# Kernel optimization log

Measured on AMD Instinct MI355X. Metric: run time of the kernel, lower is better.

Reference implementation:

```python
import jax, jax.numpy as jnp
import numpy as np


def _box_iou(a, b):
    # a: [K,4], b: [K,4] in ltrb; returns [K,K] pairwise IoU (torchvision box_iou math)
    area_a = jnp.clip(a[:, 2] - a[:, 0], 0) * jnp.clip(a[:, 3] - a[:, 1], 0)
    area_b = jnp.clip(b[:, 2] - b[:, 0], 0) * jnp.clip(b[:, 3] - b[:, 1], 0)
    lt = jnp.maximum(a[:, None, :2], b[None, :, :2])
    rb = jnp.minimum(a[:, None, 2:], b[None, :, 2:])
    wh = jnp.clip(rb - lt, 0)
    inter = wh[..., 0] * wh[..., 1]
    return inter / (area_a[:, None] + area_b[None, :] - inter + 1e-9)


def _nms_class(score, boxes, th_c, nms_th, K):
    # score: [N], boxes: [N,4]. Keep boxes with score > th_c, take top-K by score,
    # then greedy NMS suppressing lower-scored boxes with IoU >= nms_th (original keeps iou < nms_th).
    masked = jnp.where(score > th_c, score, -jnp.inf)
    top_s, idx = jax.lax.top_k(masked, K)          # descending score order
    valid = top_s > -jnp.inf
    bk = boxes[idx]                                 # [K,4]
    iou = _box_iou(bk, bk)                          # [K,K]
    order = jnp.arange(K)

    def body(alive, i):
        keep_i = alive[i]
        suppress = keep_i & (iou[i] >= nms_th) & (order > i)
        return alive & ~suppress, keep_i

    _, keep = jax.lax.scan(body, valid, order)
    return jnp.where(keep[:, None], bk, 0.0), jnp.where(keep, top_s, 0.0), keep


def decode(bboxes_in, scores_in, dboxes_xywh, conf_th, nms_th, max_num, scale_xy, scale_wh):
    B, C = bboxes_in.shape[0], scores_in.shape[1]
    K = int(max_num)
    # scale_back_batch: xywh offsets -> ltrb absolute boxes, softmax over classes
    b = jnp.transpose(bboxes_in, (0, 2, 1))                         # [B,N,4]
    xy = scale_xy * b[..., :2] * dboxes_xywh[..., 2:] + dboxes_xywh[..., :2]
    wh = jnp.exp(scale_wh * b[..., 2:]) * dboxes_xywh[..., 2:]
    ltrb = jnp.concatenate([xy - 0.5 * wh, xy + 0.5 * wh], axis=-1)  # [B,N,4]
    probs = jax.nn.softmax(jnp.transpose(scores_in, (0, 2, 1)), axis=-1)  # [B,N,C]
    cls_scores = jnp.transpose(probs[..., 1:], (0, 2, 1))            # [B,C-1,N] (skip background cls 0)

    def per_image(scores_cn, boxes_n4):
        f = jax.vmap(lambda s, t: _nms_class(s, boxes_n4, t, nms_th, K))
        return f(scores_cn, conf_th)

    bk, sk, keep = jax.vmap(per_image)(cls_scores, ltrb)  # [B,C-1,K,4], [B,C-1,K], [B,C-1,K]
    M = (C - 1) * K
    labels = jnp.arange(1, C, dtype=jnp.float32)[None, :, None] * keep.astype(jnp.float32)
    return (bk.reshape(B, M, 4), labels.reshape(B, M), sk.reshape(B, M), keep.reshape(B, M))


def setup_inputs() -> dict:
    key = jax.random.key(0)
    k0, k1, k2, k3, k4 = jax.random.split(key, 5)
    B, N, C = 32, 24564, 21
    bboxes_in = 0.5 * jax.random.normal(k0, (B, 4, N), jnp.float32)
    scores_in = jax.random.normal(k1, (B, C, N), jnp.float32)
    cxy = jax.random.uniform(k2, (1, N, 2), jnp.float32)
    dwh = jax.random.uniform(k3, (1, N, 2), jnp.float32, 0.05, 0.5)
    dboxes_xywh = jnp.concatenate([cxy, dwh], axis=-1)
    conf_th = jax.random.uniform(k4, (C - 1,), jnp.float32, 0.01, 0.05)
    return {
        'bboxes_in': bboxes_in,
        'scores_in': scores_in,
        'dboxes_xywh': dboxes_xywh,
        'conf_th': conf_th,
        'nms_th': jnp.float32(0.5),
        'max_num': 200,
        'scale_xy': 0.1,
        'scale_wh': 0.2,
    }


def reference(bboxes_in, scores_in, dboxes_xywh, conf_th, nms_th, max_num, scale_xy, scale_wh):
    # Padded, jit-compatible equivalent of the torch Decoder: per image we return
    # [(C-1)*K] slots of (boxes, labels, scores) with a boolean keep-mask; the torch
    # version returns only the kept (variable-length) entries, in the same order.
    return decode(bboxes_in, scores_in, dboxes_xywh, conf_th, nms_th, max_num, scale_xy, scale_wh)
```

## Files before the change

### kernel.cpp

```cpp
#include <hip/hip_runtime.h>
#include <math.h>

typedef unsigned int uint;
typedef unsigned short u16;
typedef unsigned long long u64;

#define NT 256
#define KTOP 200
#define CAP 256
#define CAPC 3072
#define SEGS 4
#define SEGCAP 512
#define NCLS 21
#define C1 20
#define MROWS 208
#define NSPLIT 48

__device__ __forceinline__ u64 flip64(double d) {
  u64 u = (u64)__double_as_longlong(d);
  return (u & 0x8000000000000000ULL) ? ~u : (u | 0x8000000000000000ULL);
}

__device__ __forceinline__ double unflip64(u64 k) {
  u64 u = (k & 0x8000000000000000ULL) ? (k ^ 0x8000000000000000ULL) : ~k;
  return __longlong_as_double((long long)u);
}

__device__ __forceinline__ uint q_key16(float sf) {
  float qf = (sf + 16.0f) * 4096.0f;
  qf = fmaxf(fminf(qf, 65535.0f), 1.0f);
  return (uint)qf;
}

__device__ __forceinline__ void par_walk(const uint* hist, uint* scan, u64* wm,
                                         uint* res, uint rank, int tid) {
  scan[tid] = hist[tid];
  __syncthreads();
#pragma unroll
  for (int off = 1; off < 256; off <<= 1) {
    uint v = scan[tid];
    uint a = (tid + off < 256) ? scan[tid + off] : 0u;
    __syncthreads();
    scan[tid] = v + a;
    __syncthreads();
  }
  u64 m = __ballot(scan[tid] >= rank);
  if ((tid & 63) == 0) wm[tid >> 6] = m;
  __syncthreads();
  if (tid == 0) {
    int bin = 0;
    for (int w = 3; w >= 0; --w) {
      if (wm[w]) { bin = w * 64 + (63 - __clzll(wm[w])); break; }
    }
    res[0] = (uint)bin;
    res[1] = scan[bin];
    res[2] = hist[bin];
  }
  __syncthreads();
}

__global__ __launch_bounds__(NT) void zero_ghist(uint* __restrict__ g) {
  g[(size_t)blockIdx.x * NT + threadIdx.x] = 0;
}

__global__ __launch_bounds__(NT) void prep_kernel(
    const float* __restrict__ scores, const float* __restrict__ conf_th,
    double* __restrict__ lse_out, u16* __restrict__ keys_out,
    uint* __restrict__ ghist,
    int B, int N, int npad, int perblk)
{
  __shared__ double s_logth[C1];
  __shared__ uint lhist[C1 * 256];
  int tid = threadIdx.x;
  if (tid < C1) s_logth[tid] = log((double)conf_th[tid]);
  for (int i = tid; i < C1 * 256; i += NT) lhist[i] = 0;
  __syncthreads();

  int b = blockIdx.x / NSPLIT, j = blockIdx.x - b * NSPLIT;
  int s0 = j * perblk, e0 = min(N, s0 + perblk);
  int half = (e0 - s0) >> 1;

  for (int p = tid; p < half; p += NT) {
    int n = s0 + 2 * p;
    const float* sc = scores + (size_t)b * NCLS * N + n;
    float2 v[NCLS];
    float mx0 = -INFINITY, mx1 = -INFINITY;
#pragma unroll
    for (int c = 0; c < NCLS; ++c) {
      float2 t = *reinterpret_cast<const float2*>(sc + (size_t)c * N);
      v[c] = t;
      mx0 = fmaxf(mx0, t.x);
      mx1 = fmaxf(mx1, t.y);
    }
    double a0 = 0.0, a1 = 0.0, a2 = 0.0;
    double b0 = 0.0, b1 = 0.0, b2 = 0.0;
#pragma unroll
    for (int c = 0; c < NCLS; ++c) {
      float e0f = __expf(v[c].x - mx0);
      float e1f = __expf(v[c].y - mx1);
      if ((c % 3) == 0)      { a0 += (double)e0f; b0 += (double)e1f; }
      else if ((c % 3) == 1) { a1 += (double)e0f; b1 += (double)e1f; }
      else                   { a2 += (double)e0f; b2 += (double)e1f; }
    }
    double lse0 = (double)mx0 + log(a0 + a1 + a2);
    double lse1 = (double)mx1 + log(b0 + b1 + b2);
    double2 lw; lw.x = lse0; lw.y = lse1;
    reinterpret_cast<double2*>(lse_out + (size_t)b * N + n)[0] = lw;

#pragma unroll
    for (int c = 0; c < C1; ++c) {
      double s0d = (double)v[c + 1].x - lse0;
      double s1d = (double)v[c + 1].y - lse1;
      uint k0 = 0, k1 = 0;
      if (s0d > s_logth[c]) k0 = q_key16((float)s0d);
      if (s1d > s_logth[c]) k1 = q_key16((float)s1d);
      *reinterpret_cast<uint*>(keys_out + ((size_t)b * C1 + c) * npad + n)
          = k0 | (k1 << 16);
      if (k0) atomicAdd(&lhist[c * 256 + (k0 >> 8)], 1u);
      if (k1) atomicAdd(&lhist[c * 256 + (k1 >> 8)], 1u);
    }
  }
  if (j == NSPLIT - 1 && npad > N) {
    int pad = npad - N;
    for (int t = tid; t < pad * C1; t += NT) {
      int c = t / pad, n = N + (t - c * pad);
      keys_out[((size_t)b * C1 + c) * npad + n] = 0;
    }
  }
  __syncthreads();
  for (int i = tid; i < C1 * 256; i += NT) {
    uint v2 = lhist[i];
    if (v2) atomicAdd(&ghist[((size_t)b * C1 + (i >> 8)) * 256 + (i & 255)], v2);
  }
}

__global__ __launch_bounds__(NT) void collect_kernel(
    const u16* __restrict__ keys, const uint* __restrict__ ghist,
    uint4* __restrict__ L0cnt, uint* __restrict__ cand, uint* __restrict__ cnts,
    int npad)
{
  int blk = blockIdx.x;
  int task = blk >> 2, seg = blk & (SEGS - 1);
  int tid = threadIdx.x, lane = tid & 63;
  __shared__ uint sL, sCnt0, sCnt;

  if (tid < 64) {
    uint4 h = reinterpret_cast<const uint4*>(ghist + (size_t)task * 256)[tid];
    uint s = h.x + h.y + h.z + h.w;
    uint suf = s;
#pragma unroll
    for (int off = 1; off < 64; off <<= 1) {
      uint o = (uint)__shfl_down((int)suf, off);
      if (lane + off < 64) suf += o;
    }
    uint total = (uint)__shfl((int)suf, 0);
    uint sn = (uint)__shfl_down((int)suf, 1);
    if (lane == 63) sn = 0;
    uint c3 = h.w + sn, c2 = c3 + h.z, c1 = c2 + h.y, c0 = c1 + h.x;
    uint binoff, cnt, abv;
    if (c3 >= KTOP)      { binoff = 3; cnt = c3; abv = c3 - h.w; }
    else if (c2 >= KTOP) { binoff = 2; cnt = c2; abv = c2 - h.z; }
    else if (c1 >= KTOP) { binoff = 1; cnt = c1; abv = c1 - h.y; }
    else                 { binoff = 0; cnt = c0; abv = c0 - h.x; }
    uint L0v, cnt0v, abovev;
    if (total < KTOP) {
      L0v = 1u; cnt0v = total; abovev = 0u;
    } else {
      u64 m = __ballot(suf >= KTOP);
      int l = 63 - __clzll(m);
      uint bo = (uint)__shfl((int)binoff, l);
      cnt0v = (uint)__shfl((int)cnt, l);
      abovev = (uint)__shfl((int)abv, l);
      L0v = ((uint)(4 * l) + bo) << 8;
    }
    if (lane == 0) {
      sL = L0v; sCnt0 = cnt0v;
      if (seg == 0) L0cnt[task] = make_uint4(L0v, cnt0v, abovev, total);
    }
  }
  if (tid == NT - 1) sCnt = 0;
  __syncthreads();

  uint L = sL, cnt0 = sCnt0;
  if (cnt0 > CAPC) { if (tid == 0) cnts[blk] = 0; return; }

  const u16* krow = keys + (size_t)task * npad;
  const uint4* krow8 = reinterpret_cast<const uint4*>(krow);
  int nv8 = npad >> 3;
  int per8 = (nv8 + SEGS - 1) >> 2;
  int s8 = seg * per8, e8 = min(nv8, s8 + per8);
  uint* myc = cand + ((size_t)task * SEGS + seg) * SEGCAP;

  for (int i = s8 + tid; i < e8; i += NT) {
    uint4 kv = krow8[i];
    uint base = (uint)(i << 3);
    uint ks[8] = { kv.x & 0xFFFFu, kv.x >> 16, kv.y & 0xFFFFu, kv.y >> 16,
                   kv.z & 0xFFFFu, kv.z >> 16, kv.w & 0xFFFFu, kv.w >> 16 };
#pragma unroll
    for (int comp = 0; comp < 8; ++comp) {
      uint k = ks[comp];
      bool f = (k >= L);
      u64 m = __ballot(f);
      if (m) {
        uint nb = (uint)__popcll(m);
        uint wb = 0;
        if (lane == 0) wb = atomicAdd(&sCnt, nb);
        wb = (uint)__shfl((int)wb, 0);
        if (f) {
          uint pos = wb + (uint)__popcll(m & ((1ULL << lane) - 1ULL));
          if (pos < SEGCAP) myc[pos] = (k << 15) | (base + comp);
        }
      }
    }
  }
  __syncthreads();
  if (tid == 0) cnts[blk] = sCnt;
}

__global__ __launch_bounds__(NT) void final_kernel(
    const u16* __restrict__ keys, const uint4* __restrict__ L0cnt,
    const uint* __restrict__ candg, const uint* __restrict__ cnts,
    const float* __restrict__ scores, const double* __restrict__ lse,
    const float* __restrict__ bboxes, const float* __restrict__ dboxes,
    const float* __restrict__ scale_xy_p, const float* __restrict__ scale_wh_p,
    const float* __restrict__ nms_th_p,
    float* __restrict__ out, int B, int N, int npad)
{
  int task = blockIdx.x;
  int b = task / C1, c = task - b * C1;
  int tid = threadIdx.x, lane = tid & 63, wav = tid >> 6;
  const u16* krow = keys + (size_t)task * npad;
  int nv8 = npad >> 3;

  __shared__ uint cand[CAPC];
  __shared__ uint histB[256];
  __shared__ uint scanB[256];
  __shared__ u64 wmB[4];
  __shared__ uint res3[4];
  __shared__ uint scq[SEGS];
  __shared__ int si[CAP];
  __shared__ u64 sC[CAP];
  __shared__ u64 skid[CAP];
  __shared__ float4 sbx[CAP];
  __shared__ float4 sbox[MROWS];
  __shared__ float sar[MROWS];
  __shared__ u64 smaskT[13][64];
  __shared__ u64 saliveW[4];
  __shared__ uint sCnt, sCnt2;

  uint4 w0 = L0cnt[task];
  uint cnt0 = w0.y;
  if (tid < SEGS) scq[tid] = cnts[task * SEGS + tid];
  if (tid == 0) { sCnt = 0; sCnt2 = 0; }
  if (tid < MROWS) { sbox[tid] = make_float4(0.f, 0.f, 0.f, 0.f); sar[tid] = 0.f; }
  __syncthreads();
  bool slow = (cnt0 > CAPC) ||
              (scq[0] > SEGCAP) || (scq[1] > SEGCAP) ||
              (scq[2] > SEGCAP) || (scq[3] > SEGCAP);

  uint pref = w0.x >> 8, above = w0.z, rank = KTOP - w0.z;
  uint cnt;

  if (!slow) {
    uint off1 = scq[0], off2 = off1 + scq[1], off3 = off2 + scq[2];
    cnt = off3 + scq[3];
    const uint* cg = candg + (size_t)task * SEGS * SEGCAP;
    for (int j = tid; j < (int)scq[0]; j += NT) cand[j] = cg[j];
    for (int j = tid; j < (int)scq[1]; j += NT) cand[off1 + j] = cg[SEGCAP + j];
    for (int j = tid; j < (int)scq[2]; j += NT) cand[off2 + j] = cg[2 * SEGCAP + j];
    for (int j = tid; j < (int)scq[3]; j += NT) cand[off3 + j] = cg[3 * SEGCAP + j];
    __syncthreads();
  } else {
    const uint4* krow8 = reinterpret_cast<const uint4*>(krow);
    histB[tid] = 0;
    __syncthreads();
    for (int i = tid; i < nv8; i += NT) {
      uint4 kv = krow8[i];
      uint ks[8] = { kv.x & 0xFFFFu, kv.x >> 16, kv.y & 0xFFFFu, kv.y >> 16,
                     kv.z & 0xFFFFu, kv.z >> 16, kv.w & 0xFFFFu, kv.w >> 16 };
#pragma unroll
      for (int comp = 0; comp < 8; ++comp) {
        uint k = ks[comp];
        if ((k >> 8) == pref) atomicAdd(&histB[k & 255u], 1u);
      }
    }
    __syncthreads();
    par_walk(histB, scanB, wmB, res3, rank, tid);
    uint Ts = (pref << 8) | res3[0];
    for (int i = tid; i < nv8; i += NT) {
      uint4 kv = krow8[i];
      uint base = (uint)(i << 3);
      uint ks[8] = { kv.x & 0xFFFFu, kv.x >> 16, kv.y & 0xFFFFu, kv.y >> 16,
                     kv.z & 0xFFFFu, kv.z >> 16, kv.w & 0xFFFFu, kv.w >> 16 };
#pragma unroll
      for (int comp = 0; comp < 8; ++comp) {
        uint k = ks[comp];
        bool f = (k >= Ts);
        u64 m = __ballot(f);
        if (m) {
          uint nb = (uint)__popcll(m);
          uint wb = 0;
          if (lane == 0) wb = atomicAdd(&sCnt, nb);
          wb = (uint)__shfl((int)wb, 0);
          if (f) {
            uint pos = wb + (uint)__popcll(m & ((1ULL << lane) - 1ULL));
            if (pos < CAPC) cand[pos] = (k << 15) | (base + comp);
          }
        }
      }
    }
    __syncthreads();
    cnt = min(sCnt, (uint)CAPC);
  }

  uint cntF;
  if (cnt <= CAP) {
    for (int p = tid; p < (int)cnt; p += NT) si[p] = (int)(cand[p] & 0x7FFFu);
    __syncthreads();
    cntF = cnt;
  } else {
    histB[tid] = 0;
    __syncthreads();
    for (int p = tid; p < (int)cnt; p += NT) {
      uint k = cand[p] >> 15;
      if ((k >> 8) == pref) atomicAdd(&histB[k & 255u], 1u);
    }
    __syncthreads();
    par_walk(histB, scanB, wmB, res3, rank, tid);
    uint T = (pref << 8) | res3[0];
    for (int p = tid; p < (int)cnt; p += NT) {
      uint cd = cand[p];
      if ((cd >> 15) >= T) {
        uint q = atomicAdd(&sCnt2, 1u);
        if (q < CAP) si[q] = (int)(cd & 0x7FFFu);
      }
    }
    __syncthreads();
    cntF = min(sCnt2, (uint)CAP);
  }

  int valid_cnt = (int)min(cntF, (uint)KTOP);

  {
    float sxy = *scale_xy_p, swh = *scale_wh_p;
    int p = tid;
    u64 C;
    if (p < (int)cntF) {
      int n = si[p];
      double s = (double)scores[((size_t)b * NCLS + (c + 1)) * N + n] - lse[(size_t)b * N + n];
      u64 f = flip64(s);
      C = (f & ~0x7FFFULL) | (u64)(32767 - n);
      const float* bb = bboxes + (size_t)b * 4 * N + n;
      float bx = bb[0];
      float by = bb[(size_t)N];
      float bw = bb[2 * (size_t)N];
      float bh = bb[3 * (size_t)N];
      float4 d = reinterpret_cast<const float4*>(dboxes)[n];
      float x = sxy * bx * d.z + d.x;
      float y = sxy * by * d.w + d.y;
      float w = expf(swh * bw) * d.z;
      float h = expf(swh * bh) * d.w;
      sbx[p] = make_float4(x - 0.5f * w, y - 0.5f * h, x + 0.5f * w, y + 0.5f * h);
    } else {
      C = (u64)p;
      sbx[p] = make_float4(0.f, 0.f, 0.f, 0.f);
    }
    sC[p] = C;
  }
  __syncthreads();

  {
    u64 kp = sC[tid];
    int r = 0;
#pragma unroll 8
    for (int jj = 0; jj < CAP; ++jj) r += (sC[jj] > kp) ? 1 : 0;
    if (tid < (int)cntF && r < KTOP) {
      skid[r] = kp;
      float4 bx = sbx[tid];
      sbox[r] = bx;
      sar[r] = fmaxf(bx.z - bx.x, 0.f) * fmaxf(bx.w - bx.y, 0.f);
    }
  }
  __syncthreads();

  float nth = *nms_th_p;

  {
    float4 jb0 = sbox[lane], jb1 = sbox[lane + 64], jb2 = sbox[lane + 128];
    float4 jb3 = (lane + 192 < MROWS) ? sbox[lane + 192]
                                      : make_float4(0.f, 0.f, 0.f, 0.f);
    float ja0 = sar[lane], ja1 = sar[lane + 64], ja2 = sar[lane + 128],
          ja3 = (lane + 192 < MROWS) ? sar[lane + 192] : 0.f;
    for (int w = wav; w < 13; w += 4) {
      u64 word = 0;
      int r0 = w * 16;
#pragma unroll
      for (int rr = 0; rr < 16; ++rr) {
        int r = r0 + rr;
        float4 rb = sbox[r];
        float ra = sar[r];
        uint nib = 0;
#define IOU_BIT(K, JB, JA) { \
        int j = lane + 64 * (K); \
        float xx1 = fmaxf(rb.x, JB.x), yy1 = fmaxf(rb.y, JB.y); \
        float xx2 = fminf(rb.z, JB.z), yy2 = fminf(rb.w, JB.w); \
        float ww = fmaxf(xx2 - xx1, 0.f), hh = fmaxf(yy2 - yy1, 0.f); \
        float inter = ww * hh; \
        float den = ((ra + JA) - inter) + 1e-9f; \
        if ((inter >= nth * den) && (j > r)) nib |= 1u << (K); }
        IOU_BIT(0, jb0, ja0) IOU_BIT(1, jb1, ja1)
        IOU_BIT(2, jb2, ja2) IOU_BIT(3, jb3, ja3)
#undef IOU_BIT
        word |= (u64)nib << (rr * 4);
      }
      smaskT[w][lane] = word;
    }
  }
  __syncthreads();

  if (tid < 64) {
    u64 mm[13];
#pragma unroll
    for (int w = 0; w < 13; ++w) mm[w] = smaskT[w][lane];
    uint av = 0;
#pragma unroll
    for (int k = 0; k < 4; ++k)
      if (lane + 64 * k < valid_cnt) av |= 1u << k;
#define STEP(i) { \
    u64 bm = __ballot((lane == ((i) & 63)) && ((av >> ((i) >> 6)) & 1u)); \
    if (bm) av &= ~((uint)((mm[(i) >> 4] >> (((i) & 15) * 4)) & 0xFULL)); }
#define S4(i)  STEP(i) STEP((i)+1) STEP((i)+2) STEP((i)+3)
#define S16(i) S4(i) S4((i)+4) S4((i)+8) S4((i)+12)
#define S64(i) S16(i) S16((i)+16) S16((i)+32) S16((i)+48)
    S64(0) S64(64) S64(128) S16(192)
#undef S64
#undef S16
#undef S4
#undef STEP
#pragma unroll
    for (int k = 0; k < 4; ++k) {
      u64 bb2 = __ballot((av >> k) & 1u);
      if (lane == 0) saliveW[k] = bb2;
    }
  }
  __syncthreads();

  size_t M = (size_t)C1 * KTOP;
  float* out_boxes  = out;
  float* out_labels = out + (size_t)B * M * 4;
  float* out_scores = out_labels + (size_t)B * M;
  float* out_keep   = out_scores + (size_t)B * M;
  if (tid < KTOP) {
    size_t slot = ((size_t)b * C1 + c) * KTOP + tid;
    bool kept = (tid < valid_cnt) && ((saliveW[tid >> 6] >> (tid & 63)) & 1ULL);
    float4 bx = kept ? sbox[tid] : make_float4(0.f, 0.f, 0.f, 0.f);
    reinterpret_cast<float4*>(out_boxes)[slot] = bx;
    out_labels[slot] = kept ? (float)(c + 1) : 0.0f;
    out_scores[slot] = kept ? (float)exp(unflip64(skid[tid])) : 0.0f;
    out_keep[slot]   = kept ? 1.0f : 0.0f;
  }
}

extern "C" void kernel_launch(void* const* d_in, const int* in_sizes, int n_in,
                              void* d_out, int out_size, void* d_ws, size_t ws_size,
                              hipStream_t stream) {
  const float* bboxes   = (const float*)d_in[0];
  const float* scores   = (const float*)d_in[1];
  const float* dboxes   = (const float*)d_in[2];
  const float* conf_th  = (const float*)d_in[3];
  const float* nms_th   = (const float*)d_in[4];
  const float* scale_xy = (const float*)d_in[6];
  const float* scale_wh = (const float*)d_in[7];

  int N = in_sizes[2] / 4;
  int B = in_sizes[0] / (4 * N);
  int npad = (N + 7) & ~7;

  char* ws = (char*)d_ws;
  size_t off = 0;
  double* lse     = (double*)(ws + off); off += (size_t)B * N * 8;
  u16*    keys    = (u16*)   (ws + off); off += (size_t)B * C1 * npad * 2;
  uint*   ghist   = (uint*)  (ws + off); off += (size_t)B * C1 * 256 * 4;
  uint4*  L0cnt   = (uint4*) (ws + off); off += (size_t)B * C1 * 16;
  uint*   cand    = (uint*)  (ws + off); off += (size_t)B * C1 * SEGS * SEGCAP * 4;
  uint*   cnts    = (uint*)  (ws + off);

  zero_ghist<<<B * C1, NT, 0, stream>>>(ghist);

  int perblk = ((N + NSPLIT - 1) / NSPLIT + 1) & ~1;
  prep_kernel<<<B * NSPLIT, NT, 0, stream>>>(
      scores, conf_th, lse, keys, ghist, B, N, npad, perblk);

  collect_kernel<<<B * C1 * SEGS, NT, 0, stream>>>(
      keys, ghist, L0cnt, cand, cnts, npad);

  final_kernel<<<B * C1, NT, 0, stream>>>(
      keys, L0cnt, cand, cnts, scores, lse, bboxes, dboxes,
      scale_xy, scale_wh, nms_th, (float*)d_out, B, N, npad);
}
```

Before: 93.55 us.

## Split final kernel into top-K selection and NMS mask-resolve kernels, enlarge candidate caps

Splits the monolithic final kernel into a top-K selection kernel that writes sorted keys and boxes to workspace, and a separate kernel that builds the IoU mask and resolves greedy NMS. Each kernel needs less shared memory, which could raise occupancy. The candidate buffer caps are also raised so the slow fallback path is taken less often. The cost is an extra launch, a global round trip for the top-K data, and a larger LDS footprint for the cand array in the top-K kernel.

```diff
diff --git a/kernel.cpp b/kernel.cpp
--- a/kernel.cpp
+++ b/kernel.cpp
@@ -8,9 +8,9 @@
 #define NT 256
 #define KTOP 200
 #define CAP 256
-#define CAPC 3072
+#define CAPC 6144
 #define SEGS 4
-#define SEGCAP 512
+#define SEGCAP 1280
 #define NCLS 21
 #define C1 20
 #define MROWS 208
@@ -217,18 +217,18 @@
   if (tid == 0) cnts[blk] = sCnt;
 }
 
-__global__ __launch_bounds__(NT) void final_kernel(
+__global__ __launch_bounds__(NT) void topk_kernel(
     const u16* __restrict__ keys, const uint4* __restrict__ L0cnt,
     const uint* __restrict__ candg, const uint* __restrict__ cnts,
     const float* __restrict__ scores, const double* __restrict__ lse,
     const float* __restrict__ bboxes, const float* __restrict__ dboxes,
     const float* __restrict__ scale_xy_p, const float* __restrict__ scale_wh_p,
-    const float* __restrict__ nms_th_p,
-    float* __restrict__ out, int B, int N, int npad)
+    u64* __restrict__ tkeys, float4* __restrict__ tbox, uint* __restrict__ tcnt,
+    int B, int N, int npad)
 {
   int task = blockIdx.x;
   int b = task / C1, c = task - b * C1;
-  int tid = threadIdx.x, lane = tid & 63, wav = tid >> 6;
+  int tid = threadIdx.x, lane = tid & 63;
   const u16* krow = keys + (size_t)task * npad;
   int nv8 = npad >> 3;
 
@@ -240,19 +240,13 @@
   __shared__ uint scq[SEGS];
   __shared__ int si[CAP];
   __shared__ u64 sC[CAP];
-  __shared__ u64 skid[CAP];
   __shared__ float4 sbx[CAP];
-  __shared__ float4 sbox[MROWS];
-  __shared__ float sar[MROWS];
-  __shared__ u64 smaskT[13][64];
-  __shared__ u64 saliveW[4];
   __shared__ uint sCnt, sCnt2;
 
   uint4 w0 = L0cnt[task];
   uint cnt0 = w0.y;
   if (tid < SEGS) scq[tid] = cnts[task * SEGS + tid];
   if (tid == 0) { sCnt = 0; sCnt2 = 0; }
-  if (tid < MROWS) { sbox[tid] = make_float4(0.f, 0.f, 0.f, 0.f); sar[tid] = 0.f; }
   __syncthreads();
   bool slow = (cnt0 > CAPC) ||
               (scq[0] > SEGCAP) || (scq[1] > SEGCAP) ||
@@ -338,8 +332,6 @@
     __syncthreads();
     cntF = min(sCnt2, (uint)CAP);
   }
-
-  int valid_cnt = (int)min(cntF, (uint)KTOP);
 
   {
     float sxy = *scale_xy_p, swh = *scale_wh_p;
@@ -374,16 +366,38 @@
     int r = 0;
 #pragma unroll 8
     for (int jj = 0; jj < CAP; ++jj) r += (sC[jj] > kp) ? 1 : 0;
-    if (tid < (int)cntF && r < KTOP) {
-      skid[r] = kp;
-      float4 bx = sbx[tid];
-      sbox[r] = bx;
-      sar[r] = fmaxf(bx.z - bx.x, 0.f) * fmaxf(bx.w - bx.y, 0.f);
-    }
-  }
-  __syncthreads();
-
+    if (r < KTOP) {
+      tkeys[(size_t)task * KTOP + r] = kp;
+      tbox[(size_t)task * KTOP + r] = sbx[tid];
+    }
+  }
+  if (tid == 0) tcnt[task] = min(cntF, (uint)KTOP);
+}
+
+__global__ __launch_bounds__(NT) void maskresolve_kernel(
+    const u64* __restrict__ tkeys, const float4* __restrict__ tbox,
+    const uint* __restrict__ tcnt, const float* __restrict__ nms_th_p,
+    float* __restrict__ out, int B)
+{
+  int task = blockIdx.x;
+  int b = task / C1, c = task - b * C1;
+  int tid = threadIdx.x, lane = tid & 63, wav = tid >> 6;
+
+  __shared__ float4 sbox[MROWS];
+  __shared__ float sar[MROWS];
+  __shared__ u64 smaskT[13][64];
+  __shared__ u64 saliveW[4];
+
+  int valid = (int)tcnt[task];
   float nth = *nms_th_p;
+
+  if (tid < MROWS) {
+    float4 bx = (tid < valid) ? tbox[(size_t)task * KTOP + tid]
+                              : make_float4(0.f, 0.f, 0.f, 0.f);
+    sbox[tid] = bx;
+    sar[tid] = fmaxf(bx.z - bx.x, 0.f) * fmaxf(bx.w - bx.y, 0.f);
+  }
+  __syncthreads();
 
   {
     float4 jb0 = sbox[lane], jb1 = sbox[lane + 64], jb2 = sbox[lane + 128];
@@ -425,7 +439,7 @@
     uint av = 0;
 #pragma unroll
     for (int k = 0; k < 4; ++k)
-      if (lane + 64 * k < valid_cnt) av |= 1u << k;
+      if (lane + 64 * k < valid) av |= 1u << k;
 #define STEP(i) { \
     u64 bm = __ballot((lane == ((i) & 63)) && ((av >> ((i) >> 6)) & 1u)); \
     if (bm) av &= ~((uint)((mm[(i) >> 4] >> (((i) & 15) * 4)) & 0xFULL)); }
@@ -452,11 +466,11 @@
   float* out_keep   = out_scores + (size_t)B * M;
   if (tid < KTOP) {
     size_t slot = ((size_t)b * C1 + c) * KTOP + tid;
-    bool kept = (tid < valid_cnt) && ((saliveW[tid >> 6] >> (tid & 63)) & 1ULL);
+    bool kept = (tid < valid) && ((saliveW[tid >> 6] >> (tid & 63)) & 1ULL);
     float4 bx = kept ? sbox[tid] : make_float4(0.f, 0.f, 0.f, 0.f);
     reinterpret_cast<float4*>(out_boxes)[slot] = bx;
     out_labels[slot] = kept ? (float)(c + 1) : 0.0f;
-    out_scores[slot] = kept ? (float)exp(unflip64(skid[tid])) : 0.0f;
+    out_scores[slot] = kept ? (float)exp(unflip64(tkeys[(size_t)task * KTOP + tid])) : 0.0f;
     out_keep[slot]   = kept ? 1.0f : 0.0f;
   }
 }
@@ -483,7 +497,10 @@
   uint*   ghist   = (uint*)  (ws + off); off += (size_t)B * C1 * 256 * 4;
   uint4*  L0cnt   = (uint4*) (ws + off); off += (size_t)B * C1 * 16;
   uint*   cand    = (uint*)  (ws + off); off += (size_t)B * C1 * SEGS * SEGCAP * 4;
-  uint*   cnts    = (uint*)  (ws + off);
+  uint*   cnts    = (uint*)  (ws + off); off += (size_t)B * C1 * SEGS * 4;
+  u64*    tkeys   = (u64*)   (ws + off); off += (size_t)B * C1 * KTOP * 8;
+  float4* tbox    = (float4*)(ws + off); off += (size_t)B * C1 * KTOP * 16;
+  uint*   tcnt    = (uint*)  (ws + off);
 
   zero_ghist<<<B * C1, NT, 0, stream>>>(ghist);
 
@@ -494,7 +511,10 @@
   collect_kernel<<<B * C1 * SEGS, NT, 0, stream>>>(
       keys, ghist, L0cnt, cand, cnts, npad);
 
-  final_kernel<<<B * C1, NT, 0, stream>>>(
+  topk_kernel<<<B * C1, NT, 0, stream>>>(
       keys, L0cnt, cand, cnts, scores, lse, bboxes, dboxes,
-      scale_xy, scale_wh, nms_th, (float*)d_out, B, N, npad);
-}
+      scale_xy, scale_wh, tkeys, tbox, tcnt, B, N, npad);
+
+  maskresolve_kernel<<<B * C1, NT, 0, stream>>>(
+      tkeys, tbox, tcnt, nms_th, (float*)d_out, B);
+}
```

After: 97.31 us. 1.04x slower.
